# Optimization experiments

Measured on AMD Instinct MI355X. Metric: run time of the kernel, lower is better.

The kernel has to match this reference:

```python
import jax, jax.numpy as jnp
import numpy as np


def _delta(x, window):
    # x: [B, T, D]; edge-replicate pad by `window` frames on each side,
    # then weighted antisymmetric finite difference: sum_j (x[t+j]-x[t-j])/(2j).
    B, T, D = x.shape
    pad = jnp.concatenate(
        [jnp.repeat(x[:, :1, :], window, axis=1), x, jnp.repeat(x[:, -1:, :], window, axis=1)],
        axis=1,
    )  # [B, T+2W, D]
    z = jnp.zeros_like(x)
    for j in range(1, window + 1):  # tiny fixed loop over window taps
        z = z + (pad[:, window + j: window + j + T, :] - pad[:, window - j: window - j + T, :]) / (2.0 * j)
    return z


def setup_inputs() -> dict:
    key = jax.random.key(0)
    inp = jax.random.normal(key, (32, 4096, 256), dtype=jnp.float32)
    return {"inp": inp, "window": 2}


def reference(inp, window):
    delta = _delta(inp, window)
    double_delta = _delta(delta, window)
    return jnp.concatenate([inp, delta, double_delta], axis=2)  # [B, T, 3D]
```

## Files before the change

### kernel.cpp

```cpp
#include <hip/hip_runtime.h>


#define TT   4096
#define D4   64
#define O4   192
#define TRUN 32

__device__ __forceinline__ float4 dcomb(const float4 p1, const float4 m1,
                                        const float4 p2, const float4 m2) {
    float4 r;
    r.x = (p1.x - m1.x) * 0.5f + (p2.x - m2.x) * 0.25f;
    r.y = (p1.y - m1.y) * 0.5f + (p2.y - m2.y) * 0.25f;
    r.z = (p1.z - m1.z) * 0.5f + (p2.z - m2.z) * 0.25f;
    r.w = (p1.w - m1.w) * 0.5f + (p2.w - m2.w) * 0.25f;
    return r;
}

__device__ __forceinline__ int clampT(int s) {
    return s < 0 ? 0 : (s > TT - 1 ? TT - 1 : s);
}

__global__ __launch_bounds__(256) void delta_layer_kernel(
        const float* __restrict__ x, float* __restrict__ out) {
    int idx = blockIdx.x * 256 + threadIdx.x;
    int d4  = idx & (D4 - 1);
    int seg = idx >> 6;
    int t0  = (seg & (TT / TRUN - 1)) * TRUN;
    int b   = seg >> 7;

    const float4* xb = reinterpret_cast<const float4*>(x) + b * TT * D4 + d4;

    auto ldc = [&](int r) -> float4 { return xb[clampT(r) * D4]; };
    auto deltaAt = [&](int r) -> float4 {
        return dcomb(ldc(r + 1), ldc(r - 1), ldc(r + 2), ldc(r - 2));
    };

    float4 dm2 = deltaAt(clampT(t0 - 2));
    float4 dm1 = deltaAt(clampT(t0 - 1));
    float4 dc  = deltaAt(t0);
    float4 dp1 = deltaAt(clampT(t0 + 1));
    float4 dp2 = deltaAt(clampT(t0 + 2));
    float4 x0 = ldc(t0),     x1 = ldc(t0 + 1), x2 = ldc(t0 + 2);
    float4 x3 = ldc(t0 + 3), x4 = ldc(t0 + 4);

    float4* ob = reinterpret_cast<float4*>(out) + (b * TT + t0) * O4 + d4;

    #pragma unroll
    for (int tt = 0; tt < TRUN; ++tt) {
        int t = t0 + tt;
        ob[0]      = x0;
        ob[D4]     = dc;
        ob[2 * D4] = dcomb(dp1, dm1, dp2, dm2);

        float4 xn = ldc(t + 5);
        float4 dn;
        if (t + 3 <= TT - 1) {
            dn = dcomb(x4, x2, xn, x1);
        } else {
            dn = dp2;
        }
        dm2 = dm1; dm1 = dc; dc = dp1; dp1 = dp2; dp2 = dn;
        x0 = x1; x1 = x2; x2 = x3; x3 = x4; x4 = xn;
        ob += O4;
    }
}

extern "C" void kernel_launch(void* const* d_in, const int* in_sizes, int n_in,
                              void* d_out, int out_size, void* d_ws, size_t ws_size,
                              hipStream_t stream) {
    const float* x = (const float*)d_in[0];
    float* out = (float*)d_out;
    int nthreads = (in_sizes[0] / 256 / TRUN) * D4;
    int blocks = (nthreads + 255) / 256;
    delta_layer_kernel<<<blocks, 256, 0, stream>>>(x, out);
}
```

Baseline: 492.1 us.

## Compute one time step per thread with nine-tap stencil and block swizzle

Replaces the per-thread 32-step sliding window with one output row per thread. Each interior thread loads nine neighbouring rows directly and uses a clamped path only at sequence edges. Block indices are swizzled in groups of eight to spread the memory streams. This gives far more parallelism and avoids serial dependency chains, but each input row is now read about nine times and has to be served from cache.

```diff
diff --git a/kernel.cpp b/kernel.cpp
--- a/kernel.cpp
+++ b/kernel.cpp
@@ -4,7 +4,6 @@
 #define TT   4096
 #define D4   64
 #define O4   192
-#define TRUN 32
 
 __device__ __forceinline__ float4 dcomb(const float4 p1, const float4 m1,
                                         const float4 p2, const float4 m2) {
@@ -22,46 +21,58 @@
 
 __global__ __launch_bounds__(256) void delta_layer_kernel(
         const float* __restrict__ x, float* __restrict__ out) {
-    int idx = blockIdx.x * 256 + threadIdx.x;
+    int bid = blockIdx.x;
+    int swz = (gridDim.x & 7) == 0
+                  ? (bid & 7) * (gridDim.x >> 3) + (bid >> 3)
+                  : bid;
+
+    int idx = swz * 256 + (int)threadIdx.x;
     int d4  = idx & (D4 - 1);
-    int seg = idx >> 6;
-    int t0  = (seg & (TT / TRUN - 1)) * TRUN;
-    int b   = seg >> 7;
+    int g   = idx >> 6;
+    int t   = g & (TT - 1);
+    int b   = g >> 12;
 
-    const float4* xb = reinterpret_cast<const float4*>(x) + b * TT * D4 + d4;
+    const float4* xr = reinterpret_cast<const float4*>(x)
+                       + (size_t)g * D4 + d4;
+    float4* ob = reinterpret_cast<float4*>(out)
+                 + (size_t)g * O4 + d4;
 
-    auto ldc = [&](int r) -> float4 { return xb[clampT(r) * D4]; };
-    auto deltaAt = [&](int r) -> float4 {
-        return dcomb(ldc(r + 1), ldc(r - 1), ldc(r + 2), ldc(r - 2));
-    };
+    if (t >= 4 && t <= TT - 5) {
+        float4 xm4 = xr[-4 * D4];
+        float4 xm3 = xr[-3 * D4];
+        float4 xm2 = xr[-2 * D4];
+        float4 xm1 = xr[-1 * D4];
+        float4 x0  = xr[0];
+        float4 xp1 = xr[1 * D4];
+        float4 xp2 = xr[2 * D4];
+        float4 xp3 = xr[3 * D4];
+        float4 xp4 = xr[4 * D4];
 
-    float4 dm2 = deltaAt(clampT(t0 - 2));
-    float4 dm1 = deltaAt(clampT(t0 - 1));
-    float4 dc  = deltaAt(t0);
-    float4 dp1 = deltaAt(clampT(t0 + 1));
-    float4 dp2 = deltaAt(clampT(t0 + 2));
-    float4 x0 = ldc(t0),     x1 = ldc(t0 + 1), x2 = ldc(t0 + 2);
-    float4 x3 = ldc(t0 + 3), x4 = ldc(t0 + 4);
+        float4 dm2 = dcomb(xm1, xm3, x0,  xm4);
+        float4 dm1 = dcomb(x0,  xm2, xp1, xm3);
+        float4 d0  = dcomb(xp1, xm1, xp2, xm2);
+        float4 dp1 = dcomb(xp2, x0,  xp3, xm1);
+        float4 dp2 = dcomb(xp3, xp1, xp4, x0);
 
-    float4* ob = reinterpret_cast<float4*>(out) + (b * TT + t0) * O4 + d4;
+        ob[0]      = x0;
+        ob[D4]     = d0;
+        ob[2 * D4] = dcomb(dp1, dm1, dp2, dm2);
+    } else {
+        const float4* xb = reinterpret_cast<const float4*>(x)
+                           + (size_t)b * TT * D4 + d4;
+        auto ldc = [&](int r) -> float4 { return xb[clampT(r) * D4]; };
+        auto deltaAt = [&](int r) -> float4 {
+            return dcomb(ldc(r + 1), ldc(r - 1), ldc(r + 2), ldc(r - 2));
+        };
+        float4 dm2 = deltaAt(clampT(t - 2));
+        float4 dm1 = deltaAt(clampT(t - 1));
+        float4 d0  = deltaAt(t);
+        float4 dp1 = deltaAt(clampT(t + 1));
+        float4 dp2 = deltaAt(clampT(t + 2));
 
-    #pragma unroll
-    for (int tt = 0; tt < TRUN; ++tt) {
-        int t = t0 + tt;
-        ob[0]      = x0;
-        ob[D4]     = dc;
+        ob[0]      = ldc(t);
+        ob[D4]     = d0;
         ob[2 * D4] = dcomb(dp1, dm1, dp2, dm2);
-
-        float4 xn = ldc(t + 5);
-        float4 dn;
-        if (t + 3 <= TT - 1) {
-            dn = dcomb(x4, x2, xn, x1);
-        } else {
-            dn = dp2;
-        }
-        dm2 = dm1; dm1 = dc; dc = dp1; dp1 = dp2; dp2 = dn;
-        x0 = x1; x1 = x2; x2 = x3; x3 = x4; x4 = xn;
-        ob += O4;
     }
 }
 
@@ -70,7 +81,7 @@
                               hipStream_t stream) {
     const float* x = (const float*)d_in[0];
     float* out = (float*)d_out;
-    int nthreads = (in_sizes[0] / 256 / TRUN) * D4;
+    int nthreads = in_sizes[0] / 4;
     int blocks = (nthreads + 255) / 256;
     delta_layer_kernel<<<blocks, 256, 0, stream>>>(x, out);
 }
```

After: 515.4 us. +4.7%, slower.
